# Kernel optimization log

Hardware: AMD Instinct MI355X
Metric: run time of the kernel (lower is better)

The kernel has to match this reference:

```python
import jax, jax.numpy as jnp
import numpy as np

B, NN, DEG = 64, 256, 8
N = B * NN
E = N * DEG
IN_N, IN_E = 128, 16
TOOL, PROC = 16, 12
TP = TOOL * PROC
H1 = 384

def _lin(key, i, o, s=0.05):
    k1, k2 = jax.random.split(key)
    return (jax.random.normal(k1, (i, o), jnp.float32) * s,
            jax.random.normal(k2, (o,), jnp.float32) * s)

def setup_inputs():
    ks = jax.random.split(jax.random.key(0), 40)
    inp = {}
    inp["ns"] = jax.random.normal(ks[0], (N, IN_N), jnp.float32)
    inp["es"] = jax.random.normal(ks[1], (E, IN_E), jnp.float32)
    inp["dm"] = jax.random.normal(ks[2], (N, NN), jnp.float32)
    inp["mask_fv"] = (jax.random.uniform(ks[3], (N, TP)) > 0.3).astype(jnp.float32)
    dst = jnp.repeat(jnp.arange(N, dtype=jnp.int32), DEG)  # fixed in-degree DEG
    src = (dst // NN) * NN + jax.random.randint(ks[4], (E,), 0, NN, dtype=jnp.int32)
    inp["src"], inp["dst"] = src, dst
    sizes = [(IN_N, H1), (H1 + 32, H1), (H1, TP)]
    for i, (cin, cout) in enumerate(sizes, 1):
        inp[f"Wm{i}"], inp[f"bm{i}"] = _lin(ks[5 + 3 * i], 2 * cin + IN_E, cin)
        inp[f"Wu{i}"], inp[f"bu{i}"] = _lin(ks[6 + 3 * i], 5 * cin, cout)
        inp[f"bng{i}"] = jnp.ones((cout,), jnp.float32)
        inp[f"bnb{i}"] = jnp.zeros((cout,), jnp.float32)
        inp[f"Wx{i}"], inp[f"bx{i}"] = _lin(ks[7 + 3 * i], cout, cout)
    inp["W1"], inp["b1"] = _lin(ks[20], NN, 64)
    inp["W2"], inp["b2"] = _lin(ks[21], 64, 32)
    inp["W3"], inp["b3"] = _lin(ks[22], NN, 64)
    inp["W4"], inp["b4"] = _lin(ks[23], 64, NN)
    return inp

def pna_conv(src, dst, h, e, Wm, bm, Wu, bu, bng, bnb, Wx, bx, relu_out):
    # DGL PNAConvTower: msg = M(cat(h_src, h_dst, e)); aggregate mean/max/sum/std per dst node;
    # U(cat(h, aggs)); BatchNorm (training stats); mixing Linear + LeakyReLU(0.01).
    cin = h.shape[1]
    msg = h[src] @ Wm[:cin] + h[dst] @ Wm[cin:2 * cin] + e @ Wm[2 * cin:] + bm  # [E, cin]
    cnt = jax.ops.segment_sum(jnp.ones((msg.shape[0],), msg.dtype), dst, N)[:, None]
    s = jax.ops.segment_sum(msg, dst, N)
    mean = s / cnt
    mx = jax.ops.segment_max(msg, dst, N)
    msq = jax.ops.segment_sum(msg * msg, dst, N) / cnt
    std = jnp.sqrt(jax.nn.relu(msq - mean * mean) + 1e-30)
    u = jnp.concatenate([h, mean, mx, s, std], axis=-1) @ Wu + bu  # [N, cout]
    u = (u - u.mean(0)) / jnp.sqrt(u.var(0) + 1e-5) * bng + bnb  # BatchNorm1d, training mode
    out = jax.nn.leaky_relu(u @ Wx + bx, 0.01)  # mixing layer
    return jax.nn.relu(out) if relu_out else out

def reference(ns, es, dm, mask_fv, Wm1, bm1, Wu1, bu1, bng1, bnb1, Wx1, bx1, Wm2, bm2, Wu2, bu2, bng2, bnb2, Wx2, bx2, Wm3, bm3, Wu3, bu3, bng3, bnb3, Wx3, bx3, W1, b1, W2, b2, W3, b3, W4, b4, src, dst):
    d2 = (dm @ W1 + b1) @ W2 + b2  # [N, 32]
    h1 = pna_conv(src, dst, ns, es, Wm1, bm1, Wu1, bu1, bng1, bnb1, Wx1, bx1, True)
    h2 = pna_conv(src, dst, jnp.concatenate([h1, d2], -1), es, Wm2, bm2, Wu2, bu2, bng2, bnb2, Wx2, bx2, True)
    h3 = pna_conv(src, dst, h2, es, Wm3, bm3, Wu3, bu3, bng3, bnb3, Wx3, bx3, False)  # [N, TP]
    nm = h3.max(-1).reshape(B, NN)
    g = jax.nn.sigmoid(jax.nn.relu(nm @ W3 + b3) @ W4 + b4)  # [B, NN]
    feat = (g.reshape(N, 1) * h3).reshape(B, -1)  # [B, NN*TP]
    feat = jnp.where(mask_fv.reshape(B, -1) == 0, -1e5, feat)
    return jax.nn.softmax(feat, -1)
```

## Files before the change

### kernel.cpp

```cpp
#include <hip/hip_runtime.h>
#include <hip/hip_bf16.h>

#define NNODE 16384

typedef short v8s __attribute__((ext_vector_type(8)));
typedef float v4f __attribute__((ext_vector_type(4)));
typedef unsigned short us16;

__device__ __forceinline__ us16 f2bf(float v) {
    unsigned u = __float_as_uint(v);
    unsigned r = (u + 0x7FFF + ((u >> 16) & 1)) >> 16;
    return (us16)r;
}
__device__ __forceinline__ float bf2f(us16 s) {
    return __uint_as_float(((unsigned)s) << 16);
}

template<int EPI, int OUT, int ACC, int BM>
__global__ __launch_bounds__(256, 4)
void mgemm5(const us16* __restrict__ Ah, const us16* __restrict__ Al,
            int ldA, int K,
            const us16* __restrict__ Bh, const us16* __restrict__ Bl, int KC,
            const float* __restrict__ CfIn, int ldCin,
            float* __restrict__ Cf, us16* __restrict__ Ch, us16* __restrict__ Cl,
            int ldC, int Ncol, const float* __restrict__ bias)
{
    constexpr int MF = BM / 32;
    __shared__ __align__(16) us16 AhS[BM * 64];
    __shared__ __align__(16) us16 AlS[BM * 64];
    const int bm = blockIdx.x * BM;
    const int bn = blockIdx.y * 64;
    const int tid = threadIdx.x;
    const int lane = tid & 63, wid = tid >> 6;
    const int wm = wid >> 1, wn = wid & 1;
    const int r16 = lane & 15, q = lane >> 4;
    v4f acc[MF][2];
#pragma unroll
    for (int i = 0; i < MF; i++)
#pragma unroll
        for (int j = 0; j < 2; j++) acc[i][j] = (v4f){0.f, 0.f, 0.f, 0.f};

    const int srow = tid >> 3;
    const int sc8  = tid & 7;
    const int cb0  = (bn >> 4) + wn * 2;
    const int nK = (K + 63) >> 6;
    for (int s = 0; s < nK; s++) {
        const int k0 = s << 6;
#pragma unroll
        for (int p = 0; p < BM / 32; p++) {
            int row = p * 32 + srow;
            size_t go = (size_t)(bm + row) * ldA + k0 + sc8 * 8;
            v8s hv = *(const v8s*)(const void*)(Ah + go);
            v8s lv = *(const v8s*)(const void*)(Al + go);
            int bo = row * 128 + ((sc8 * 16) ^ ((row & 7) << 4));
            *(v8s*)(void*)((char*)AhS + bo) = hv;
            *(v8s*)(void*)((char*)AlS + bo) = lv;
        }
        v8s Bfh[2][2], Bfl[2][2];
#pragma unroll
        for (int kc = 0; kc < 2; kc++) {
            int kchunk = (k0 >> 5) + kc;
#pragma unroll
            for (int nf = 0; nf < 2; nf++) {
                size_t fo = ((size_t)((cb0 + nf) * KC + kchunk) * 64 + lane) * 8;
                Bfh[kc][nf] = *(const v8s*)(const void*)(Bh + fo);
                Bfl[kc][nf] = *(const v8s*)(const void*)(Bl + fo);
            }
        }
        __syncthreads();
#pragma unroll
        for (int kc = 0; kc < 2; kc++) {
#pragma unroll
            for (int mf = 0; mf < MF; mf++) {
                int arow = wm * (BM / 2) + mf * 16 + r16;
                int ao = arow * 128 + (((kc * 64) + q * 16) ^ ((arow & 7) << 4));
                v8s ah = *(const v8s*)(const void*)((const char*)AhS + ao);
                v8s al = *(const v8s*)(const void*)((const char*)AlS + ao);
#pragma unroll
                for (int nf = 0; nf < 2; nf++) {
                    acc[mf][nf] = __builtin_amdgcn_mfma_f32_16x16x32_bf16(ah, Bfh[kc][nf], acc[mf][nf], 0, 0, 0);
                    acc[mf][nf] = __builtin_amdgcn_mfma_f32_16x16x32_bf16(al, Bfh[kc][nf], acc[mf][nf], 0, 0, 0);
                    acc[mf][nf] = __builtin_amdgcn_mfma_f32_16x16x32_bf16(ah, Bfl[kc][nf], acc[mf][nf], 0, 0, 0);
                }
            }
        }
        __syncthreads();
    }
#pragma unroll
    for (int mf = 0; mf < MF; mf++)
#pragma unroll
        for (int nf = 0; nf < 2; nf++) {
            int col = bn + wn * 32 + nf * 16 + r16;
            if (col < Ncol) {
                float bv = bias ? bias[col] : 0.f;
#pragma unroll
                for (int r = 0; r < 4; r++) {
                    int row = bm + wm * (BM / 2) + mf * 16 + q * 4 + r;
                    float v = acc[mf][nf][r] + bv;
                    if (ACC) v += CfIn[(size_t)row * ldCin + col];
                    if (EPI == 1) v = fmaxf(v, 0.f);
                    if (EPI == 2) v = (v > 0.f) ? v : 0.01f * v;
                    size_t o = (size_t)row * ldC + col;
                    if (OUT == 0) {
                        Cf[o] = v;
                    } else {
                        us16 h = f2bf(v);
                        Ch[o] = h;
                        Cl[o] = f2bf(v - bf2f(h));
                    }
                }
            }
        }
}

__global__ void prep_fr_bt(const float* __restrict__ W, int ldW,
                           us16* __restrict__ Bh, us16* __restrict__ Bl,
                           int K, int N, int KC)
{
    int idx = blockIdx.x * 256 + threadIdx.x;
    if (idx >= N * KC * 32) return;
    int e = idx & 7, lane = (idx >> 3) & 63, rem = idx >> 9;
    int kchunk = rem % KC, colblk = rem / KC;
    int n = colblk * 16 + (lane & 15);
    int k = kchunk * 32 + (lane >> 4) * 8 + e;
    float v = (k < K && n < N) ? W[(size_t)k * ldW + n] : 0.f;
    us16 h = f2bf(v);
    Bh[idx] = h;
    Bl[idx] = f2bf(v - bf2f(h));
}

__global__ void prep_fr_wu(const float* __restrict__ Wu,
                           us16* __restrict__ Bh, us16* __restrict__ Bl,
                           int cin, int cout, int KC)
{
    int idx = blockIdx.x * 256 + threadIdx.x;
    if (idx >= cout * KC * 32) return;
    int e = idx & 7, lane = (idx >> 3) & 63, rem = idx >> 9;
    int kchunk = rem % KC, colblk = rem / KC;
    int n = colblk * 16 + (lane & 15);
    int k = kchunk * 32 + (lane >> 4) * 8 + e;
    float v = 0.f;
    if (n < cout && k < 3 * cin) {
        if (k < cin)          v = Wu[(size_t)(cin + k) * cout + n] * 0.125f + Wu[(size_t)(3 * cin + k) * cout + n];
        else if (k < 2 * cin) v = Wu[(size_t)(2 * cin + (k - cin)) * cout + n];
        else                  v = Wu[(size_t)(4 * cin + (k - 2 * cin)) * cout + n];
    }
    us16 h = f2bf(v);
    Bh[idx] = h;
    Bl[idx] = f2bf(v - bf2f(h));
}

__global__ void prep_fr_wx(const float* __restrict__ Wx, const float* __restrict__ scale,
                           us16* __restrict__ Bh, us16* __restrict__ Bl,
                           int K, int N, int KC)
{
    int idx = blockIdx.x * 256 + threadIdx.x;
    if (idx >= N * KC * 32) return;
    int e = idx & 7, lane = (idx >> 3) & 63, rem = idx >> 9;
    int kchunk = rem % KC, colblk = rem / KC;
    int n = colblk * 16 + (lane & 15);
    int k = kchunk * 32 + (lane >> 4) * 8 + e;
    float v = (k < K && n < N) ? Wx[(size_t)k * N + n] * scale[k] : 0.f;
    us16 h = f2bf(v);
    Bh[idx] = h;
    Bl[idx] = f2bf(v - bf2f(h));
}

__global__ __launch_bounds__(256) void bias2p_k(const float* __restrict__ Wx,
    const float* __restrict__ bx, const float* __restrict__ shift,
    float* __restrict__ bias2, int K, int N)
{
    int n = blockIdx.x, tid = threadIdx.x;
    float s = 0.f;
    for (int k = tid; k < K; k += 256) s = fmaf(shift[k], Wx[(size_t)k * N + n], s);
    __shared__ float red[256];
    red[tid] = s; __syncthreads();
    for (int st = 128; st > 0; st >>= 1) { if (tid < st) red[tid] += red[tid + st]; __syncthreads(); }
    if (tid == 0) bias2[n] = red[0] + bx[n];
}

__global__ void prep_biasMU(const float* __restrict__ bm, const float* __restrict__ bu,
                            float* __restrict__ o, int cin, int cout)
{
    int i = blockIdx.x * 256 + threadIdx.x;
    if (i >= 2 * cin + cout) return;
    float v;
    if (i < cin)          v = 0.f;
    else if (i < 2 * cin) v = bm[i - cin];
    else                  v = bu[i - 2 * cin];
    o[i] = v;
}

__global__ void csplit_k(const float* __restrict__ src, int ldS, int w,
                         us16* __restrict__ Xh, us16* __restrict__ Xl,
                         int ldX, int offX)
{
    int idx = blockIdx.x * 256 + threadIdx.x;
    if (idx >= NNODE * w) return;
    int rrow = idx / w, c = idx - rrow * w;
    float v = src[(size_t)rrow * ldS + c];
    us16 h = f2bf(v);
    size_t o = (size_t)rrow * ldX + offX + c;
    Xh[o] = h;
    Xl[o] = f2bf(v - bf2f(h));
}

__global__ __launch_bounds__(256)
void gemm_k(const float* __restrict__ A, const float* __restrict__ Bw,
            float* __restrict__ C, int Ncol, int K, const float* __restrict__ bias)
{
    __shared__ float As[16][128];
    __shared__ float Bs[16][64];
    const int bm = blockIdx.y * 128;
    const int bn = blockIdx.x * 64;
    const int tid = threadIdx.x;
    const int tx = tid & 15, ty = tid >> 4;
    float acc[8][4];
#pragma unroll
    for (int i = 0; i < 8; i++)
#pragma unroll
        for (int j = 0; j < 4; j++) acc[i][j] = 0.f;

    for (int k0 = 0; k0 < K; k0 += 16) {
#pragma unroll
        for (int i = 0; i < 2; i++) {
            int idx = tid * 2 + i;
            int row = idx >> 2;
            int k4  = (idx & 3) << 2;
            const float* ap = A + (size_t)(bm + row) * K + k0 + k4;
            float4 v = *reinterpret_cast<const float4*>(ap);
            As[k4 + 0][row] = v.x;
            As[k4 + 1][row] = v.y;
            As[k4 + 2][row] = v.z;
            As[k4 + 3][row] = v.w;
        }
        {
            int row = tid >> 4;
            int c4  = (tid & 15) << 2;
            int gn  = bn + c4;
            float4 v;
            if (gn + 3 < Ncol) {
                v = *reinterpret_cast<const float4*>(Bw + (size_t)(k0 + row) * Ncol + gn);
            } else {
                float t0 = (gn + 0 < Ncol) ? Bw[(size_t)(k0 + row) * Ncol + gn + 0] : 0.f;
                float t1 = (gn + 1 < Ncol) ? Bw[(size_t)(k0 + row) * Ncol + gn + 1] : 0.f;
                float t2 = (gn + 2 < Ncol) ? Bw[(size_t)(k0 + row) * Ncol + gn + 2] : 0.f;
                float t3 = (gn + 3 < Ncol) ? Bw[(size_t)(k0 + row) * Ncol + gn + 3] : 0.f;
                v = make_float4(t0, t1, t2, t3);
            }
            *reinterpret_cast<float4*>(&Bs[row][c4]) = v;
        }
        __syncthreads();
#pragma unroll
        for (int kk = 0; kk < 16; kk++) {
            float a0[8], b0[4];
#pragma unroll
            for (int i = 0; i < 8; i++) a0[i] = As[kk][ty * 8 + i];
#pragma unroll
            for (int j = 0; j < 4; j++) b0[j] = Bs[kk][tx * 4 + j];
#pragma unroll
            for (int i = 0; i < 8; i++)
#pragma unroll
                for (int j = 0; j < 4; j++) acc[i][j] = fmaf(a0[i], b0[j], acc[i][j]);
        }
        __syncthreads();
    }
#pragma unroll
    for (int i = 0; i < 8; i++) {
        int r = bm + ty * 8 + i;
#pragma unroll
        for (int j = 0; j < 4; j++) {
            int c = bn + tx * 4 + j;
            if (c < Ncol) C[(size_t)r * Ncol + c] = acc[i][j] + (bias ? bias[c] : 0.f);
        }
    }
}

__global__ __launch_bounds__(256)
void agg2_k(const float* __restrict__ H2, const float* __restrict__ es,
            const int* __restrict__ src, const float* __restrict__ Wme,
            us16* __restrict__ Xh, us16* __restrict__ Xl,
            int cin, int ldH, int ldX, int offX)
{
    const int g = blockIdx.x;
    const int c0 = blockIdx.y * 64;
    const int qz = blockIdx.z;
    const int tid = threadIdx.x;
    const int nl = tid >> 6, c = tid & 63;
    const int cc = c0 + c;
    const bool act = cc < cin;
    __shared__ float esl[4][128];
    __shared__ int srcl[512];
    {
        int e0 = g * 2048 + qz * 512;
        for (int i = tid; i < 512; i += 256) srcl[i] = src[e0 + i] - g * 256;
    }
    float wreg[16];
#pragma unroll
    for (int j = 0; j < 16; j++) wreg[j] = act ? Wme[j * cin + cc] : 0.f;
    __syncthreads();
    const float* Hsrc = H2 + (size_t)(g * 256) * ldH + c0;
    const float* Hdst = H2 + (size_t)(g * 256) * ldH + cin + c0;
    for (int i = 0; i < 16; i++) {
        const int vl = qz * 64 + i * 4 + nl;
        {
            const float* ep = es + (size_t)(g * 256 + vl) * 128;
            esl[nl][c] = ep[c];
            esl[nl][64 + c] = ep[64 + c];
        }
        __syncthreads();
        if (act) {
            float hd = Hdst[(size_t)vl * ldH + c];
            float sum = 0.f, sq = 0.f, mx = -INFINITY;
#pragma unroll
            for (int e = 0; e < 8; e++) {
                int sl = srcl[(i * 4 + nl) * 8 + e];
                float m = hd + Hsrc[(size_t)sl * ldH + c];
                float4 e0 = *(const float4*)&esl[nl][e * 16 + 0];
                float4 e1 = *(const float4*)&esl[nl][e * 16 + 4];
                float4 e2 = *(const float4*)&esl[nl][e * 16 + 8];
                float4 e3 = *(const float4*)&esl[nl][e * 16 + 12];
                m = fmaf(e0.x, wreg[0], m);  m = fmaf(e0.y, wreg[1], m);
                m = fmaf(e0.z, wreg[2], m);  m = fmaf(e0.w, wreg[3], m);
                m = fmaf(e1.x, wreg[4], m);  m = fmaf(e1.y, wreg[5], m);
                m = fmaf(e1.z, wreg[6], m);  m = fmaf(e1.w, wreg[7], m);
                m = fmaf(e2.x, wreg[8], m);  m = fmaf(e2.y, wreg[9], m);
                m = fmaf(e2.z, wreg[10], m); m = fmaf(e2.w, wreg[11], m);
                m = fmaf(e3.x, wreg[12], m); m = fmaf(e3.y, wreg[13], m);
                m = fmaf(e3.z, wreg[14], m); m = fmaf(e3.w, wreg[15], m);
                sum += m;
                sq = fmaf(m, m, sq);
                mx = fmaxf(mx, m);
            }
            float mean = sum * 0.125f, msq = sq * 0.125f;
            float stdv = sqrtf(fmaxf(msq - mean * mean, 0.f) + 1e-30f);
            size_t o = (size_t)(g * 256 + vl) * ldX + offX + cc;
            us16 h;
            h = f2bf(sum);  Xh[o] = h;            Xl[o] = f2bf(sum - bf2f(h));
            h = f2bf(mx);   Xh[o + cin] = h;      Xl[o + cin] = f2bf(mx - bf2f(h));
            h = f2bf(stdv); Xh[o + 2 * cin] = h;  Xl[o + 2 * cin] = f2bf(stdv - bf2f(h));
        }
        __syncthreads();
    }
}

__global__ void bnstats1s_k(const us16* __restrict__ uh, const us16* __restrict__ ul,
                            float* __restrict__ part, int cout)
{
    int c = threadIdx.x;
    if (c >= cout) return;
    int r0 = blockIdx.x * 256;
    float s = 0.f, q = 0.f;
    for (int r = r0; r < r0 + 256; r++) {
        size_t o = (size_t)r * cout + c;
        float v = bf2f(uh[o]) + bf2f(ul[o]);
        s += v;
        q = fmaf(v, v, q);
    }
    part[(size_t)blockIdx.x * cout + c] = s;
    part[(size_t)(64 + blockIdx.x) * cout + c] = q;
}

__global__ void bnstats2_k(const float* __restrict__ part, const float* __restrict__ bng,
                           const float* __restrict__ bnb, float* __restrict__ scale,
                           float* __restrict__ shift, int cout)
{
    int c = threadIdx.x;
    if (c >= cout) return;
    float s = 0.f, q = 0.f;
    for (int b = 0; b < 64; b++) { s += part[(size_t)b * cout + c]; q += part[(size_t)(64 + b) * cout + c]; }
    float mean = s / 16384.f;
    float var  = q / 16384.f - mean * mean;
    float sc   = bng[c] / sqrtf(var + 1e-5f);
    scale[c] = sc;
    shift[c] = bnb[c] - mean * sc;
}

__global__ void rowmax_k(const float* __restrict__ h3, float* __restrict__ nm)
{
    int wave = threadIdx.x >> 6;
    int lane = threadIdx.x & 63;
    int node = blockIdx.x * 4 + wave;
    const float* row = h3 + (size_t)node * 192;
    float m = -INFINITY;
    for (int t = lane; t < 192; t += 64) m = fmaxf(m, row[t]);
#pragma unroll
    for (int off = 32; off > 0; off >>= 1) m = fmaxf(m, __shfl_down(m, off, 64));
    if (lane == 0) nm[node] = m;
}

__global__ __launch_bounds__(256) void g_k(const float* __restrict__ nm,
    const float* __restrict__ W3, const float* __restrict__ b3,
    const float* __restrict__ W4, const float* __restrict__ b4,
    float* __restrict__ g)
{
    __shared__ float row[256];
    __shared__ float t1[64];
    int b = blockIdx.x, tid = threadIdx.x;
    row[tid] = nm[b * 256 + tid];
    __syncthreads();
    if (tid < 64) {
        float a = b3[tid];
        for (int k = 0; k < 256; k++) a = fmaf(row[k], W3[k * 64 + tid], a);
        t1[tid] = fmaxf(a, 0.f);
    }
    __syncthreads();
    float a = b4[tid];
    for (int j = 0; j < 64; j++) a = fmaf(t1[j], W4[j * 256 + tid], a);
    g[b * 256 + tid] = 1.f / (1.f + expf(-a));
}

__global__ __launch_bounds__(256) void sm1_k(const float* __restrict__ mask,
    const float* __restrict__ g, const float* __restrict__ h3, float* __restrict__ part)
{
    int b = blockIdx.x, s = blockIdx.y, tid = threadIdx.x;
    float l[24];
#pragma unroll
    for (int t = 0; t < 24; t++) {
        int i = s * 6144 + t * 256 + tid;
        size_t idx = (size_t)b * 49152 + i;
        float mk = mask[idx];
        l[t] = (mk == 0.f) ? -1e5f : g[b * 256 + i / 192] * h3[idx];
    }
    float m = -INFINITY;
#pragma unroll
    for (int t = 0; t < 24; t++) m = fmaxf(m, l[t]);
    __shared__ float red[256];
    red[tid] = m; __syncthreads();
    for (int st = 128; st > 0; st >>= 1) { if (tid < st) red[tid] = fmaxf(red[tid], red[tid + st]); __syncthreads(); }
    m = red[0]; __syncthreads();
    float z = 0.f;
#pragma unroll
    for (int t = 0; t < 24; t++) z += expf(l[t] - m);
    red[tid] = z; __syncthreads();
    for (int st = 128; st > 0; st >>= 1) { if (tid < st) red[tid] += red[tid + st]; __syncthreads(); }
    if (tid == 0) { part[(b * 8 + s) * 2] = m; part[(b * 8 + s) * 2 + 1] = red[0]; }
}

__global__ void sm2_k(const float* __restrict__ part, float* __restrict__ mz)
{
    int b = threadIdx.x;
    if (b >= 64) return;
    float M = -INFINITY;
    for (int s = 0; s < 8; s++) M = fmaxf(M, part[(b * 8 + s) * 2]);
    float Z = 0.f;
    for (int s = 0; s < 8; s++) Z += part[(b * 8 + s) * 2 + 1] * expf(part[(b * 8 + s) * 2] - M);
    mz[b * 2] = M;
    mz[b * 2 + 1] = 1.f / Z;
}

__global__ __launch_bounds__(256) void sm3_k(const float* __restrict__ mask,
    const float* __restrict__ g, const float* __restrict__ h3,
    const float* __restrict__ mz, float* __restrict__ out)
{
    int b = blockIdx.x, s = blockIdx.y, tid = threadIdx.x;
    float M = mz[b * 2], invZ = mz[b * 2 + 1];
#pragma unroll
    for (int t = 0; t < 24; t++) {
        int i = s * 6144 + t * 256 + tid;
        size_t idx = (size_t)b * 49152 + i;
        float mk = mask[idx];
        float v = (mk == 0.f) ? -1e5f : g[b * 256 + i / 192] * h3[idx];
        out[idx] = expf(v - M) * invZ;
    }
}

extern "C" void kernel_launch(void* const* d_in, const int* in_sizes, int n_in,
                              void* d_out, int out_size, void* d_ws, size_t ws_size,
                              hipStream_t stream)
{
    const float* ns   = (const float*)d_in[0];
    const float* es   = (const float*)d_in[1];
    const float* dm   = (const float*)d_in[2];
    const float* mask = (const float*)d_in[3];
    const int*   src  = (const int*)d_in[4];
    const float* Wm1 = (const float*)d_in[6],  *bm1 = (const float*)d_in[7];
    const float* Wu1 = (const float*)d_in[8],  *bu1 = (const float*)d_in[9];
    const float* bng1= (const float*)d_in[10], *bnb1= (const float*)d_in[11];
    const float* Wx1 = (const float*)d_in[12], *bx1 = (const float*)d_in[13];
    const float* Wm2 = (const float*)d_in[14], *bm2 = (const float*)d_in[15];
    const float* Wu2 = (const float*)d_in[16], *bu2 = (const float*)d_in[17];
    const float* bng2= (const float*)d_in[18], *bnb2= (const float*)d_in[19];
    const float* Wx2 = (const float*)d_in[20], *bx2 = (const float*)d_in[21];
    const float* Wm3 = (const float*)d_in[22], *bm3 = (const float*)d_in[23];
    const float* Wu3 = (const float*)d_in[24], *bu3 = (const float*)d_in[25];
    const float* bng3= (const float*)d_in[26], *bnb3= (const float*)d_in[27];
    const float* Wx3 = (const float*)d_in[28], *bx3 = (const float*)d_in[29];
    const float* W1 = (const float*)d_in[30], *b1 = (const float*)d_in[31];
    const float* W2 = (const float*)d_in[32], *b2 = (const float*)d_in[33];
    const float* W3 = (const float*)d_in[34], *b3 = (const float*)d_in[35];
    const float* W4 = (const float*)d_in[36], *b4 = (const float*)d_in[37];
    float* out = (float*)d_out;

    const int N = NNODE;
    char* base = (char*)d_ws;
    size_t off = 0;
    auto alloc = [&](size_t bytes) -> void* {
        void* p = base + off;
        off = (off + bytes + 255) & ~(size_t)255;
        return p;
    };
    us16* Xh = (us16*)alloc((size_t)N * 1728 * 2);
    us16* Xl = (us16*)alloc((size_t)N * 1728 * 2);
    float* H2   = (float*)alloc((size_t)N * 1216 * 4);
    us16* uh = (us16*)alloc((size_t)N * 384 * 2);
    us16* ul = (us16*)alloc((size_t)N * 384 * 2);
    float* h3b  = (float*)alloc((size_t)N * 192 * 4);
    float* d2f  = (float*)alloc((size_t)N * 32 * 4);
    float* part = (float*)alloc((size_t)128 * 384 * 4);
    float* scale= (float*)alloc(384 * 4);
    float* shift= (float*)alloc(384 * 4);
    float* bias2= (float*)alloc(384 * 4);
    float* biasMU1 = (float*)alloc(640 * 4);
    float* biasMU2 = (float*)alloc(1216 * 4);
    float* biasMU3 = (float*)alloc(960 * 4);
    float* nm   = (float*)alloc((size_t)N * 4);
    float* gbuf = (float*)alloc((size_t)N * 4);
    float* smp  = (float*)alloc(64 * 8 * 2 * 4);
    float* smz  = (float*)alloc(64 * 2 * 4);
    auto aw = [&](size_t elems) -> us16* { return (us16*)alloc(elems * 2); };
    us16 *BM1h = aw((size_t)640 * 128),   *BM1l = aw((size_t)640 * 128);
    us16 *BA1h = aw((size_t)384 * 384),   *BA1l = aw((size_t)384 * 384);
    us16 *BX1h = aw((size_t)384 * 384),   *BX1l = aw((size_t)384 * 384);
    us16 *BM2h = aw((size_t)1216 * 448),  *BM2l = aw((size_t)1216 * 448);
    us16 *BA2h = aw((size_t)384 * 1280),  *BA2l = aw((size_t)384 * 1280);
    us16 *BX2h = aw((size_t)384 * 384),   *BX2l = aw((size_t)384 * 384);
    us16 *BM3h = aw((size_t)960 * 384),   *BM3l = aw((size_t)960 * 384);
    us16 *BA3h = aw((size_t)192 * 1152),  *BA3l = aw((size_t)192 * 1152);
    us16 *BX3h = aw((size_t)192 * 192),   *BX3l = aw((size_t)192 * 192);

    auto gp = [](size_t n) { return dim3((unsigned)((n + 255) / 256)); };
    auto fsec = [](us16* b, int c0, int KC) { return b + (size_t)(c0 / 16) * KC * 512; };

    prep_fr_bt<<<gp((size_t)128 * 128), 256, 0, stream>>>(Wm1,             128, fsec(BM1h, 0, 4),   fsec(BM1l, 0, 4),   128, 128, 4);
    prep_fr_bt<<<gp((size_t)128 * 128), 256, 0, stream>>>(Wm1 + 128 * 128, 128, fsec(BM1h, 128, 4), fsec(BM1l, 128, 4), 128, 128, 4);
    prep_fr_bt<<<gp((size_t)384 * 128), 256, 0, stream>>>(Wu1,             384, fsec(BM1h, 256, 4), fsec(BM1l, 256, 4), 128, 384, 4);
    prep_fr_wu<<<gp((size_t)384 * 384), 256, 0, stream>>>(Wu1, BA1h, BA1l, 128, 384, 12);
    prep_fr_bt<<<gp((size_t)416 * 448), 256, 0, stream>>>(Wm2,             416, fsec(BM2h, 0, 14),   fsec(BM2l, 0, 14),   416, 416, 14);
    prep_fr_bt<<<gp((size_t)416 * 448), 256, 0, stream>>>(Wm2 + 416 * 416, 416, fsec(BM2h, 416, 14), fsec(BM2l, 416, 14), 416, 416, 14);
    prep_fr_bt<<<gp((size_t)384 * 448), 256, 0, stream>>>(Wu2,             384, fsec(BM2h, 832, 14), fsec(BM2l, 832, 14), 416, 384, 14);
    prep_fr_wu<<<gp((size_t)384 * 1280), 256, 0, stream>>>(Wu2, BA2h, BA2l, 416, 384, 40);
    prep_fr_bt<<<gp((size_t)384 * 384), 256, 0, stream>>>(Wm3,             384, fsec(BM3h, 0, 12),   fsec(BM3l, 0, 12),   384, 384, 12);
    prep_fr_bt<<<gp((size_t)384 * 384), 256, 0, stream>>>(Wm3 + 384 * 384, 384, fsec(BM3h, 384, 12), fsec(BM3l, 384, 12), 384, 384, 12);
    prep_fr_bt<<<gp((size_t)192 * 384), 256, 0, stream>>>(Wu3,             192, fsec(BM3h, 768, 12), fsec(BM3l, 768, 12), 384, 192, 12);
    prep_fr_wu<<<gp((size_t)192 * 1152), 256, 0, stream>>>(Wu3, BA3h, BA3l, 384, 192, 36);
    prep_biasMU<<<gp(640), 256, 0, stream>>>(bm1, bu1, biasMU1, 128, 384);
    prep_biasMU<<<gp(1216), 256, 0, stream>>>(bm2, bu2, biasMU2, 416, 384);
    prep_biasMU<<<gp(960), 256, 0, stream>>>(bm3, bu3, biasMU3, 384, 192);

    csplit_k<<<gp((size_t)N * 128), 256, 0, stream>>>(ns, 128, 128, Xh, Xl, 512, 0);

    gemm_k<<<dim3(1, 128), 256, 0, stream>>>(dm, W1, H2, 64, 256, b1);
    gemm_k<<<dim3(1, 128), 256, 0, stream>>>(H2, W2, d2f, 32, 64, b2);

    mgemm5<0, 0, 0, 128><<<dim3(128, 10), 256, 0, stream>>>(Xh, Xl, 512, 128, BM1h, BM1l, 4,
        nullptr, 0, H2, nullptr, nullptr, 640, 640, biasMU1);
    agg2_k<<<dim3(64, 2, 4), 256, 0, stream>>>(H2, es, src, Wm1 + 2 * 128 * 128, Xh, Xl, 128, 640, 512, 128);
    mgemm5<0, 1, 1, 128><<<dim3(128, 6), 256, 0, stream>>>(Xh + 128, Xl + 128, 512, 384, BA1h, BA1l, 12,
        H2 + 256, 640, nullptr, uh, ul, 384, 384, nullptr);
    bnstats1s_k<<<64, 384, 0, stream>>>(uh, ul, part, 384);
    bnstats2_k<<<1, 384, 0, stream>>>(part, bng1, bnb1, scale, shift, 384);
    prep_fr_wx<<<gp((size_t)384 * 384), 256, 0, stream>>>(Wx1, scale, BX1h, BX1l, 384, 384, 12);
    bias2p_k<<<384, 256, 0, stream>>>(Wx1, bx1, shift, bias2, 384, 384);
    mgemm5<1, 1, 0, 128><<<dim3(128, 6), 256, 0, stream>>>(uh, ul, 384, 384, BX1h, BX1l, 12,
        nullptr, 0, nullptr, Xh, Xl, 1728, 384, bias2);
    csplit_k<<<gp((size_t)N * 32), 256, 0, stream>>>(d2f, 32, 32, Xh, Xl, 1728, 384);

    mgemm5<0, 0, 0, 128><<<dim3(128, 19), 256, 0, stream>>>(Xh, Xl, 1728, 416, BM2h, BM2l, 14,
        nullptr, 0, H2, nullptr, nullptr, 1216, 1216, biasMU2);
    agg2_k<<<dim3(64, 7, 4), 256, 0, stream>>>(H2, es, src, Wm2 + 2 * 416 * 416, Xh, Xl, 416, 1216, 1728, 416);
    mgemm5<0, 1, 1, 128><<<dim3(128, 6), 256, 0, stream>>>(Xh + 416, Xl + 416, 1728, 1248, BA2h, BA2l, 40,
        H2 + 832, 1216, nullptr, uh, ul, 384, 384, nullptr);
    bnstats1s_k<<<64, 384, 0, stream>>>(uh, ul, part, 384);
    bnstats2_k<<<1, 384, 0, stream>>>(part, bng2, bnb2, scale, shift, 384);
    prep_fr_wx<<<gp((size_t)384 * 384), 256, 0, stream>>>(Wx2, scale, BX2h, BX2l, 384, 384, 12);
    bias2p_k<<<384, 256, 0, stream>>>(Wx2, bx2, shift, bias2, 384, 384);
    mgemm5<1, 1, 0, 128><<<dim3(128, 6), 256, 0, stream>>>(uh, ul, 384, 384, BX2h, BX2l, 12,
        nullptr, 0, nullptr, Xh, Xl, 1536, 384, bias2);

    mgemm5<0, 0, 0, 128><<<dim3(128, 15), 256, 0, stream>>>(Xh, Xl, 1536, 384, BM3h, BM3l, 12,
        nullptr, 0, H2, nullptr, nullptr, 960, 960, biasMU3);
    agg2_k<<<dim3(64, 6, 4), 256, 0, stream>>>(H2, es, src, Wm3 + 2 * 384 * 384, Xh, Xl, 384, 960, 1536, 384);
    mgemm5<0, 1, 1, 64><<<dim3(256, 3), 256, 0, stream>>>(Xh + 384, Xl + 384, 1536, 1152, BA3h, BA3l, 36,
        H2 + 768, 960, nullptr, uh, ul, 192, 192, nullptr);
    bnstats1s_k<<<64, 384, 0, stream>>>(uh, ul, part, 192);
    bnstats2_k<<<1, 384, 0, stream>>>(part, bng3, bnb3, scale, shift, 192);
    prep_fr_wx<<<gp((size_t)192 * 192), 256, 0, stream>>>(Wx3, scale, BX3h, BX3l, 192, 192, 6);
    bias2p_k<<<192, 256, 0, stream>>>(Wx3, bx3, shift, bias2, 192, 192);
    mgemm5<2, 0, 0, 64><<<dim3(256, 3), 256, 0, stream>>>(uh, ul, 192, 192, BX3h, BX3l, 6,
        nullptr, 0, h3b, nullptr, nullptr, 192, 192, bias2);

    rowmax_k<<<N / 4, 256, 0, stream>>>(h3b, nm);
    g_k<<<64, 256, 0, stream>>>(nm, W3, b3, W4, b4, gbuf);
    sm1_k<<<dim3(64, 8), 256, 0, stream>>>(mask, gbuf, h3b, smp);
    sm2_k<<<1, 64, 0, stream>>>(smp, smz);
    sm3_k<<<dim3(64, 8), 256, 0, stream>>>(mask, gbuf, h3b, smz, out);
}
```

Before: 700.5 us.

## Widen GEMM column tiles, batch weight prep, fold dm MLP into MFMA GEMM

The MFMA GEMM gains an NB template parameter so one block covers 128 columns for the wide message GEMMs, reusing each staged A tile across more MFMAs and halving the grid's repeated A loads. Weight fragment preparation is merged into a single packed launch. W1·W2 is folded on device into one matrix so the dm projection runs as a single split-bf16 MFMA GEMM instead of two fp32 SIMT GEMMs. BN statistics use more blocks with shorter row ranges. Risks include higher register pressure from the doubled accumulators (launch bounds lowered to 3) and mode-2 descriptors that zero padding columns.

```diff
diff --git a/kernel.cpp b/kernel.cpp
--- a/kernel.cpp
+++ b/kernel.cpp
@@ -16,9 +16,9 @@
     return __uint_as_float(((unsigned)s) << 16);
 }
 
-template<int EPI, int OUT, int ACC, int BM>
-__global__ __launch_bounds__(256, 4)
-void mgemm5(const us16* __restrict__ Ah, const us16* __restrict__ Al,
+template<int EPI, int OUT, int ACC, int BM, int NB>
+__global__ __launch_bounds__(256, 3)
+void mgemm6(const us16* __restrict__ Ah, const us16* __restrict__ Al,
             int ldA, int K,
             const us16* __restrict__ Bh, const us16* __restrict__ Bl, int KC,
             const float* __restrict__ CfIn, int ldCin,
@@ -29,47 +29,54 @@
     __shared__ __align__(16) us16 AhS[BM * 64];
     __shared__ __align__(16) us16 AlS[BM * 64];
     const int bm = blockIdx.x * BM;
-    const int bn = blockIdx.y * 64;
+    const int bn0 = blockIdx.y * (64 * NB);
     const int tid = threadIdx.x;
     const int lane = tid & 63, wid = tid >> 6;
     const int wm = wid >> 1, wn = wid & 1;
     const int r16 = lane & 15, q = lane >> 4;
-    v4f acc[MF][2];
-#pragma unroll
-    for (int i = 0; i < MF; i++)
-#pragma unroll
-        for (int j = 0; j < 2; j++) acc[i][j] = (v4f){0.f, 0.f, 0.f, 0.f};
+    v4f acc[NB][MF][2];
+#pragma unroll
+    for (int b = 0; b < NB; b++)
+#pragma unroll
+        for (int i = 0; i < MF; i++)
+#pragma unroll
+            for (int j = 0; j < 2; j++) acc[b][i][j] = (v4f){0.f, 0.f, 0.f, 0.f};
 
     const int srow = tid >> 3;
     const int sc8  = tid & 7;
-    const int cb0  = (bn >> 4) + wn * 2;
+    const int cbw  = (bn0 >> 4) + wn * 2;
     const int nK = (K + 63) >> 6;
     for (int s = 0; s < nK; s++) {
         const int k0 = s << 6;
 #pragma unroll
         for (int p = 0; p < BM / 32; p++) {
             int row = p * 32 + srow;
-            size_t go = (size_t)(bm + row) * ldA + k0 + sc8 * 8;
-            v8s hv = *(const v8s*)(const void*)(Ah + go);
-            v8s lv = *(const v8s*)(const void*)(Al + go);
+            int gk = k0 + sc8 * 8;
+            v8s hv = (v8s){0,0,0,0,0,0,0,0};
+            v8s lv = (v8s){0,0,0,0,0,0,0,0};
+            if (gk < K) {
+                size_t go = (size_t)(bm + row) * ldA + gk;
+                hv = *(const v8s*)(const void*)(Ah + go);
+                lv = *(const v8s*)(const void*)(Al + go);
+            }
             int bo = row * 128 + ((sc8 * 16) ^ ((row & 7) << 4));
             *(v8s*)(void*)((char*)AhS + bo) = hv;
             *(v8s*)(void*)((char*)AlS + bo) = lv;
         }
-        v8s Bfh[2][2], Bfl[2][2];
+        __syncthreads();
 #pragma unroll
         for (int kc = 0; kc < 2; kc++) {
             int kchunk = (k0 >> 5) + kc;
-#pragma unroll
-            for (int nf = 0; nf < 2; nf++) {
-                size_t fo = ((size_t)((cb0 + nf) * KC + kchunk) * 64 + lane) * 8;
-                Bfh[kc][nf] = *(const v8s*)(const void*)(Bh + fo);
-                Bfl[kc][nf] = *(const v8s*)(const void*)(Bl + fo);
-            }
-        }
-        __syncthreads();
-#pragma unroll
-        for (int kc = 0; kc < 2; kc++) {
+            v8s bfh[NB][2], bfl[NB][2];
+#pragma unroll
+            for (int nb = 0; nb < NB; nb++)
+#pragma unroll
+                for (int nf = 0; nf < 2; nf++) {
+                    int colblk = cbw + nb * 4 + nf;
+                    size_t fo = ((size_t)(colblk * KC + kchunk) * 64 + lane) * 8;
+                    bfh[nb][nf] = *(const v8s*)(const void*)(Bh + fo);
+                    bfl[nb][nf] = *(const v8s*)(const void*)(Bl + fo);
+                }
 #pragma unroll
             for (int mf = 0; mf < MF; mf++) {
                 int arow = wm * (BM / 2) + mf * 16 + r16;
@@ -77,77 +84,80 @@
                 v8s ah = *(const v8s*)(const void*)((const char*)AhS + ao);
                 v8s al = *(const v8s*)(const void*)((const char*)AlS + ao);
 #pragma unroll
-                for (int nf = 0; nf < 2; nf++) {
-                    acc[mf][nf] = __builtin_amdgcn_mfma_f32_16x16x32_bf16(ah, Bfh[kc][nf], acc[mf][nf], 0, 0, 0);
-                    acc[mf][nf] = __builtin_amdgcn_mfma_f32_16x16x32_bf16(al, Bfh[kc][nf], acc[mf][nf], 0, 0, 0);
-                    acc[mf][nf] = __builtin_amdgcn_mfma_f32_16x16x32_bf16(ah, Bfl[kc][nf], acc[mf][nf], 0, 0, 0);
-                }
+                for (int nb = 0; nb < NB; nb++)
+#pragma unroll
+                    for (int nf = 0; nf < 2; nf++) {
+                        acc[nb][mf][nf] = __builtin_amdgcn_mfma_f32_16x16x32_bf16(ah, bfh[nb][nf], acc[nb][mf][nf], 0, 0, 0);
+                        acc[nb][mf][nf] = __builtin_amdgcn_mfma_f32_16x16x32_bf16(al, bfh[nb][nf], acc[nb][mf][nf], 0, 0, 0);
+                        acc[nb][mf][nf] = __builtin_amdgcn_mfma_f32_16x16x32_bf16(ah, bfl[nb][nf], acc[nb][mf][nf], 0, 0, 0);
+                    }
             }
         }
         __syncthreads();
     }
 #pragma unroll
-    for (int mf = 0; mf < MF; mf++)
-#pragma unroll
-        for (int nf = 0; nf < 2; nf++) {
-            int col = bn + wn * 32 + nf * 16 + r16;
-            if (col < Ncol) {
-                float bv = bias ? bias[col] : 0.f;
-#pragma unroll
-                for (int r = 0; r < 4; r++) {
-                    int row = bm + wm * (BM / 2) + mf * 16 + q * 4 + r;
-                    float v = acc[mf][nf][r] + bv;
-                    if (ACC) v += CfIn[(size_t)row * ldCin + col];
-                    if (EPI == 1) v = fmaxf(v, 0.f);
-                    if (EPI == 2) v = (v > 0.f) ? v : 0.01f * v;
-                    size_t o = (size_t)row * ldC + col;
-                    if (OUT == 0) {
-                        Cf[o] = v;
-                    } else {
-                        us16 h = f2bf(v);
-                        Ch[o] = h;
-                        Cl[o] = f2bf(v - bf2f(h));
+    for (int nb = 0; nb < NB; nb++)
+#pragma unroll
+        for (int mf = 0; mf < MF; mf++)
+#pragma unroll
+            for (int nf = 0; nf < 2; nf++) {
+                int col = bn0 + nb * 64 + wn * 32 + nf * 16 + r16;
+                if (col < Ncol) {
+                    float bv = bias ? bias[col] : 0.f;
+#pragma unroll
+                    for (int r = 0; r < 4; r++) {
+                        int row = bm + wm * (BM / 2) + mf * 16 + q * 4 + r;
+                        float v = acc[nb][mf][nf][r] + bv;
+                        if (ACC) v += CfIn[(size_t)row * ldCin + col];
+                        if (EPI == 1) v = fmaxf(v, 0.f);
+                        if (EPI == 2) v = (v > 0.f) ? v : 0.01f * v;
+                        size_t o = (size_t)row * ldC + col;
+                        if (OUT == 0) {
+                            Cf[o] = v;
+                        } else {
+                            us16 h = f2bf(v);
+                            Ch[o] = h;
+                            Cl[o] = f2bf(v - bf2f(h));
+                        }
                     }
                 }
             }
-        }
-}
-
-__global__ void prep_fr_bt(const float* __restrict__ W, int ldW,
-                           us16* __restrict__ Bh, us16* __restrict__ Bl,
-                           int K, int N, int KC)
-{
-    int idx = blockIdx.x * 256 + threadIdx.x;
-    if (idx >= N * KC * 32) return;
+}
+
+struct FrD {
+    const float* W;
+    us16* Bh;
+    us16* Bl;
+    int ldW, Kv, Nv, Na, KC, mode, cin, blk0;
+};
+struct FrPack { FrD d[16]; int nd; };
+
+__global__ __launch_bounds__(256) void prep_fr_all(FrPack p)
+{
+    int b = blockIdx.x;
+    int i = 0;
+    for (int j = 1; j < p.nd; j++) if (b >= p.d[j].blk0) i = j;
+    const FrD dd = p.d[i];
+    int idx = (b - dd.blk0) * 256 + threadIdx.x;
+    if (idx >= dd.Na * dd.KC * 32) return;
     int e = idx & 7, lane = (idx >> 3) & 63, rem = idx >> 9;
-    int kchunk = rem % KC, colblk = rem / KC;
-    int n = colblk * 16 + (lane & 15);
-    int k = kchunk * 32 + (lane >> 4) * 8 + e;
-    float v = (k < K && n < N) ? W[(size_t)k * ldW + n] : 0.f;
-    us16 h = f2bf(v);
-    Bh[idx] = h;
-    Bl[idx] = f2bf(v - bf2f(h));
-}
-
-__global__ void prep_fr_wu(const float* __restrict__ Wu,
-                           us16* __restrict__ Bh, us16* __restrict__ Bl,
-                           int cin, int cout, int KC)
-{
-    int idx = blockIdx.x * 256 + threadIdx.x;
-    if (idx >= cout * KC * 32) return;
-    int e = idx & 7, lane = (idx >> 3) & 63, rem = idx >> 9;
-    int kchunk = rem % KC, colblk = rem / KC;
+    int kchunk = rem % dd.KC, colblk = rem / dd.KC;
     int n = colblk * 16 + (lane & 15);
     int k = kchunk * 32 + (lane >> 4) * 8 + e;
     float v = 0.f;
-    if (n < cout && k < 3 * cin) {
-        if (k < cin)          v = Wu[(size_t)(cin + k) * cout + n] * 0.125f + Wu[(size_t)(3 * cin + k) * cout + n];
-        else if (k < 2 * cin) v = Wu[(size_t)(2 * cin + (k - cin)) * cout + n];
-        else                  v = Wu[(size_t)(4 * cin + (k - 2 * cin)) * cout + n];
+    if (dd.mode == 0) {
+        if (k < dd.Kv && n < dd.Nv) v = dd.W[(size_t)k * dd.ldW + n];
+    } else if (dd.mode == 1) {
+        int cin = dd.cin, cout = dd.Nv;
+        if (n < cout && k < 3 * cin) {
+            if (k < cin)          v = dd.W[(size_t)(cin + k) * cout + n] * 0.125f + dd.W[(size_t)(3 * cin + k) * cout + n];
+            else if (k < 2 * cin) v = dd.W[(size_t)(2 * cin + (k - cin)) * cout + n];
+            else                  v = dd.W[(size_t)(4 * cin + (k - 2 * cin)) * cout + n];
+        }
     }
     us16 h = f2bf(v);
-    Bh[idx] = h;
-    Bl[idx] = f2bf(v - bf2f(h));
+    dd.Bh[idx] = h;
+    dd.Bl[idx] = f2bf(v - bf2f(h));
 }
 
 __global__ void prep_fr_wx(const float* __restrict__ Wx, const float* __restrict__ scale,
@@ -166,6 +176,34 @@
     Bl[idx] = f2bf(v - bf2f(h));
 }
 
+__global__ void w12frag_k(const float* __restrict__ W1, const float* __restrict__ W2,
+                          us16* __restrict__ Bh, us16* __restrict__ Bl)
+{
+    int idx = blockIdx.x * 256 + threadIdx.x;
+    if (idx >= 64 * 8 * 32) return;
+    int e = idx & 7, lane = (idx >> 3) & 63, rem = idx >> 9;
+    int kchunk = rem % 8, colblk = rem / 8;
+    int n = colblk * 16 + (lane & 15);
+    int k = kchunk * 32 + (lane >> 4) * 8 + e;
+    float v = 0.f;
+    if (n < 32 && k < 256) {
+        for (int j = 0; j < 64; j++) v = fmaf(W1[(size_t)k * 64 + j], W2[(size_t)j * 32 + n], v);
+    }
+    us16 h = f2bf(v);
+    Bh[idx] = h;
+    Bl[idx] = f2bf(v - bf2f(h));
+}
+
+__global__ void bias12_k(const float* __restrict__ b1, const float* __restrict__ W2,
+                         const float* __restrict__ b2, float* __restrict__ b12)
+{
+    int n = threadIdx.x;
+    if (n >= 32) return;
+    float s = b2[n];
+    for (int j = 0; j < 64; j++) s = fmaf(b1[j], W2[(size_t)j * 32 + n], s);
+    b12[n] = s;
+}
+
 __global__ __launch_bounds__(256) void bias2p_k(const float* __restrict__ Wx,
     const float* __restrict__ bx, const float* __restrict__ shift,
     float* __restrict__ bias2, int K, int N)
@@ -189,6 +227,27 @@
     else if (i < 2 * cin) v = bm[i - cin];
     else                  v = bu[i - 2 * cin];
     o[i] = v;
+}
+
+__global__ void csplit2_k(const float* __restrict__ ns, us16* __restrict__ Xh, us16* __restrict__ Xl,
+                          const float* __restrict__ dm, us16* __restrict__ Dh, us16* __restrict__ Dl)
+{
+    int b = blockIdx.x;
+    if (b < 8192) {
+        int idx = b * 256 + threadIdx.x;
+        int rrow = idx >> 7, c = idx & 127;
+        float v = ns[idx];
+        us16 h = f2bf(v);
+        size_t o = (size_t)rrow * 512 + c;
+        Xh[o] = h;
+        Xl[o] = f2bf(v - bf2f(h));
+    } else {
+        int idx = (b - 8192) * 256 + threadIdx.x;
+        float v = dm[idx];
+        us16 h = f2bf(v);
+        Dh[idx] = h;
+        Dl[idx] = f2bf(v - bf2f(h));
+    }
 }
 
 __global__ void csplit_k(const float* __restrict__ src, int ldS, int w,
@@ -203,77 +262,6 @@
     size_t o = (size_t)rrow * ldX + offX + c;
     Xh[o] = h;
     Xl[o] = f2bf(v - bf2f(h));
-}
-
-__global__ __launch_bounds__(256)
-void gemm_k(const float* __restrict__ A, const float* __restrict__ Bw,
-            float* __restrict__ C, int Ncol, int K, const float* __restrict__ bias)
-{
-    __shared__ float As[16][128];
-    __shared__ float Bs[16][64];
-    const int bm = blockIdx.y * 128;
-    const int bn = blockIdx.x * 64;
-    const int tid = threadIdx.x;
-    const int tx = tid & 15, ty = tid >> 4;
-    float acc[8][4];
-#pragma unroll
-    for (int i = 0; i < 8; i++)
-#pragma unroll
-        for (int j = 0; j < 4; j++) acc[i][j] = 0.f;
-
-    for (int k0 = 0; k0 < K; k0 += 16) {
-#pragma unroll
-        for (int i = 0; i < 2; i++) {
-            int idx = tid * 2 + i;
-            int row = idx >> 2;
-            int k4  = (idx & 3) << 2;
-            const float* ap = A + (size_t)(bm + row) * K + k0 + k4;
-            float4 v = *reinterpret_cast<const float4*>(ap);
-            As[k4 + 0][row] = v.x;
-            As[k4 + 1][row] = v.y;
-            As[k4 + 2][row] = v.z;
-            As[k4 + 3][row] = v.w;
-        }
-        {
-            int row = tid >> 4;
-            int c4  = (tid & 15) << 2;
-            int gn  = bn + c4;
-            float4 v;
-            if (gn + 3 < Ncol) {
-                v = *reinterpret_cast<const float4*>(Bw + (size_t)(k0 + row) * Ncol + gn);
-            } else {
-                float t0 = (gn + 0 < Ncol) ? Bw[(size_t)(k0 + row) * Ncol + gn + 0] : 0.f;
-                float t1 = (gn + 1 < Ncol) ? Bw[(size_t)(k0 + row) * Ncol + gn + 1] : 0.f;
-                float t2 = (gn + 2 < Ncol) ? Bw[(size_t)(k0 + row) * Ncol + gn + 2] : 0.f;
-                float t3 = (gn + 3 < Ncol) ? Bw[(size_t)(k0 + row) * Ncol + gn + 3] : 0.f;
-                v = make_float4(t0, t1, t2, t3);
-            }
-            *reinterpret_cast<float4*>(&Bs[row][c4]) = v;
-        }
-        __syncthreads();
-#pragma unroll
-        for (int kk = 0; kk < 16; kk++) {
-            float a0[8], b0[4];
-#pragma unroll
-            for (int i = 0; i < 8; i++) a0[i] = As[kk][ty * 8 + i];
-#pragma unroll
-            for (int j = 0; j < 4; j++) b0[j] = Bs[kk][tx * 4 + j];
-#pragma unroll
-            for (int i = 0; i < 8; i++)
-#pragma unroll
-                for (int j = 0; j < 4; j++) acc[i][j] = fmaf(a0[i], b0[j], acc[i][j]);
-        }
-        __syncthreads();
-    }
-#pragma unroll
-    for (int i = 0; i < 8; i++) {
-        int r = bm + ty * 8 + i;
-#pragma unroll
-        for (int j = 0; j < 4; j++) {
-            int c = bn + tx * 4 + j;
-            if (c < Ncol) C[(size_t)r * Ncol + c] = acc[i][j] + (bias ? bias[c] : 0.f);
-        }
-    }
 }
 
 __global__ __launch_bounds__(256)
@@ -349,16 +337,16 @@
 {
     int c = threadIdx.x;
     if (c >= cout) return;
-    int r0 = blockIdx.x * 256;
+    int r0 = blockIdx.x * 64;
     float s = 0.f, q = 0.f;
-    for (int r = r0; r < r0 + 256; r++) {
+    for (int r = r0; r < r0 + 64; r++) {
         size_t o = (size_t)r * cout + c;
         float v = bf2f(uh[o]) + bf2f(ul[o]);
         s += v;
         q = fmaf(v, v, q);
     }
     part[(size_t)blockIdx.x * cout + c] = s;
-    part[(size_t)(64 + blockIdx.x) * cout + c] = q;
+    part[(size_t)(256 + blockIdx.x) * cout + c] = q;
 }
 
 __global__ void bnstats2_k(const float* __restrict__ part, const float* __restrict__ bng,
@@ -368,7 +356,7 @@
     int c = threadIdx.x;
     if (c >= cout) return;
     float s = 0.f, q = 0.f;
-    for (int b = 0; b < 64; b++) { s += part[(size_t)b * cout + c]; q += part[(size_t)(64 + b) * cout + c]; }
+    for (int b = 0; b < 256; b++) { s += part[(size_t)b * cout + c]; q += part[(size_t)(256 + b) * cout + c]; }
     float mean = s / 16384.f;
     float var  = q / 16384.f - mean * mean;
     float sc   = bng[c] / sqrtf(var + 1e-5f);
@@ -505,12 +493,15 @@
     float* H2   = (float*)alloc((size_t)N * 1216 * 4);
     us16* uh = (us16*)alloc((size_t)N * 384 * 2);
     us16* ul = (us16*)alloc((size_t)N * 384 * 2);
+    us16* dmh = (us16*)alloc((size_t)N * 256 * 2);
+    us16* dml = (us16*)alloc((size_t)N * 256 * 2);
     float* h3b  = (float*)alloc((size_t)N * 192 * 4);
     float* d2f  = (float*)alloc((size_t)N * 32 * 4);
-    float* part = (float*)alloc((size_t)128 * 384 * 4);
+    float* part = (float*)alloc((size_t)512 * 384 * 4);
     float* scale= (float*)alloc(384 * 4);
     float* shift= (float*)alloc(384 * 4);
     float* bias2= (float*)alloc(384 * 4);
+    float* b12  = (float*)alloc(32 * 4);
     float* biasMU1 = (float*)alloc(640 * 4);
     float* biasMU2 = (float*)alloc(1216 * 4);
     float* biasMU3 = (float*)alloc(960 * 4);
@@ -519,75 +510,89 @@
     float* smp  = (float*)alloc(64 * 8 * 2 * 4);
     float* smz  = (float*)alloc(64 * 2 * 4);
     auto aw = [&](size_t elems) -> us16* { return (us16*)alloc(elems * 2); };
-    us16 *BM1h = aw((size_t)640 * 128),   *BM1l = aw((size_t)640 * 128);
-    us16 *BA1h = aw((size_t)384 * 384),   *BA1l = aw((size_t)384 * 384);
-    us16 *BX1h = aw((size_t)384 * 384),   *BX1l = aw((size_t)384 * 384);
-    us16 *BM2h = aw((size_t)1216 * 448),  *BM2l = aw((size_t)1216 * 448);
-    us16 *BA2h = aw((size_t)384 * 1280),  *BA2l = aw((size_t)384 * 1280);
-    us16 *BX2h = aw((size_t)384 * 384),   *BX2l = aw((size_t)384 * 384);
-    us16 *BM3h = aw((size_t)960 * 384),   *BM3l = aw((size_t)960 * 384);
-    us16 *BA3h = aw((size_t)192 * 1152),  *BA3l = aw((size_t)192 * 1152);
-    us16 *BX3h = aw((size_t)192 * 192),   *BX3l = aw((size_t)192 * 192);
+    us16 *BM1h = aw((size_t)640 * 4 * 32),    *BM1l = aw((size_t)640 * 4 * 32);
+    us16 *BA1h = aw((size_t)384 * 12 * 32),   *BA1l = aw((size_t)384 * 12 * 32);
+    us16 *BX1h = aw((size_t)384 * 12 * 32),   *BX1l = aw((size_t)384 * 12 * 32);
+    us16 *BM2h = aw((size_t)1280 * 14 * 32),  *BM2l = aw((size_t)1280 * 14 * 32);
+    us16 *BA2h = aw((size_t)384 * 40 * 32),   *BA2l = aw((size_t)384 * 40 * 32);
+    us16 *BX2h = aw((size_t)384 * 12 * 32),   *BX2l = aw((size_t)384 * 12 * 32);
+    us16 *BM3h = aw((size_t)1024 * 12 * 32),  *BM3l = aw((size_t)1024 * 12 * 32);
+    us16 *BA3h = aw((size_t)192 * 36 * 32),   *BA3l = aw((size_t)192 * 36 * 32);
+    us16 *BX3h = aw((size_t)192 * 6 * 32),    *BX3l = aw((size_t)192 * 6 * 32);
+    us16 *B12h = aw((size_t)64 * 8 * 32),     *B12l = aw((size_t)64 * 8 * 32);
 
     auto gp = [](size_t n) { return dim3((unsigned)((n + 255) / 256)); };
     auto fsec = [](us16* b, int c0, int KC) { return b + (size_t)(c0 / 16) * KC * 512; };
 
-    prep_fr_bt<<<gp((size_t)128 * 128), 256, 0, stream>>>(Wm1,             128, fsec(BM1h, 0, 4),   fsec(BM1l, 0, 4),   128, 128, 4);
-    prep_fr_bt<<<gp((size_t)128 * 128), 256, 0, stream>>>(Wm1 + 128 * 128, 128, fsec(BM1h, 128, 4), fsec(BM1l, 128, 4), 128, 128, 4);
-    prep_fr_bt<<<gp((size_t)384 * 128), 256, 0, stream>>>(Wu1,             384, fsec(BM1h, 256, 4), fsec(BM1l, 256, 4), 128, 384, 4);
-    prep_fr_wu<<<gp((size_t)384 * 384), 256, 0, stream>>>(Wu1, BA1h, BA1l, 128, 384, 12);
-    prep_fr_bt<<<gp((size_t)416 * 448), 256, 0, stream>>>(Wm2,             416, fsec(BM2h, 0, 14),   fsec(BM2l, 0, 14),   416, 416, 14);
-    prep_fr_bt<<<gp((size_t)416 * 448), 256, 0, stream>>>(Wm2 + 416 * 416, 416, fsec(BM2h, 416, 14), fsec(BM2l, 416, 14), 416, 416, 14);
-    prep_fr_bt<<<gp((size_t)384 * 448), 256, 0, stream>>>(Wu2,             384, fsec(BM2h, 832, 14), fsec(BM2l, 832, 14), 416, 384, 14);
-    prep_fr_wu<<<gp((size_t)384 * 1280), 256, 0, stream>>>(Wu2, BA2h, BA2l, 416, 384, 40);
-    prep_fr_bt<<<gp((size_t)384 * 384), 256, 0, stream>>>(Wm3,             384, fsec(BM3h, 0, 12),   fsec(BM3l, 0, 12),   384, 384, 12);
-    prep_fr_bt<<<gp((size_t)384 * 384), 256, 0, stream>>>(Wm3 + 384 * 384, 384, fsec(BM3h, 384, 12), fsec(BM3l, 384, 12), 384, 384, 12);
-    prep_fr_bt<<<gp((size_t)192 * 384), 256, 0, stream>>>(Wu3,             192, fsec(BM3h, 768, 12), fsec(BM3l, 768, 12), 384, 192, 12);
-    prep_fr_wu<<<gp((size_t)192 * 1152), 256, 0, stream>>>(Wu3, BA3h, BA3l, 384, 192, 36);
+    FrPack pk;
+    int nd = 0, blk = 0;
+    auto addD = [&](const float* W, us16* Bh, us16* Bl, int ldW, int Kv, int Nv, int Na, int KC, int mode, int cin) {
+        pk.d[nd] = {W, Bh, Bl, ldW, Kv, Nv, Na, KC, mode, cin, blk};
+        blk += (Na * KC * 32 + 255) / 256;
+        nd++;
+    };
+    addD(Wm1,             fsec(BM1h,0,4),    fsec(BM1l,0,4),    128, 128, 128, 128, 4, 0, 0);
+    addD(Wm1 + 128*128,   fsec(BM1h,128,4),  fsec(BM1l,128,4),  128, 128, 128, 128, 4, 0, 0);
+    addD(Wu1,             fsec(BM1h,256,4),  fsec(BM1l,256,4),  384, 128, 384, 384, 4, 0, 0);
+    addD(Wu1,             BA1h, BA1l,        0,   0,   384, 384, 12, 1, 128);
+    addD(Wm2,             fsec(BM2h,0,14),   fsec(BM2l,0,14),   416, 416, 416, 416, 14, 0, 0);
+    addD(Wm2 + 416*416,   fsec(BM2h,416,14), fsec(BM2l,416,14), 416, 416, 416, 416, 14, 0, 0);
+    addD(Wu2,             fsec(BM2h,832,14), fsec(BM2l,832,14), 384, 416, 384, 384, 14, 0, 0);
+    addD(nullptr,         fsec(BM2h,1216,14),fsec(BM2l,1216,14),0,   0,   0,   64,  14, 2, 0);
+    addD(Wu2,             BA2h, BA2l,        0,   0,   384, 384, 40, 1, 416);
+    addD(Wm3,             fsec(BM3h,0,12),   fsec(BM3l,0,12),   384, 384, 384, 384, 12, 0, 0);
+    addD(Wm3 + 384*384,   fsec(BM3h,384,12), fsec(BM3l,384,12), 384, 384, 384, 384, 12, 0, 0);
+    addD(Wu3,             fsec(BM3h,768,12), fsec(BM3l,768,12), 192, 384, 192, 192, 12, 0, 0);
+    addD(nullptr,         fsec(BM3h,960,12), fsec(BM3l,960,12), 0,   0,   0,   64,  12, 2, 0);
+    addD(Wu3,             BA3h, BA3l,        0,   0,   192, 192, 36, 1, 384);
+    pk.nd = nd;
+
+    csplit2_k<<<8192 + 16384, 256, 0, stream>>>(ns, Xh, Xl, dm, dmh, dml);
+    prep_fr_all<<<blk, 256, 0, stream>>>(pk);
+    w12frag_k<<<gp(64 * 8 * 32), 256, 0, stream>>>(W1, W2, B12h, B12l);
+    bias12_k<<<1, 32, 0, stream>>>(b1, W2, b2, b12);
     prep_biasMU<<<gp(640), 256, 0, stream>>>(bm1, bu1, biasMU1, 128, 384);
     prep_biasMU<<<gp(1216), 256, 0, stream>>>(bm2, bu2, biasMU2, 416, 384);
     prep_biasMU<<<gp(960), 256, 0, stream>>>(bm3, bu3, biasMU3, 384, 192);
 
-    csplit_k<<<gp((size_t)N * 128), 256, 0, stream>>>(ns, 128, 128, Xh, Xl, 512, 0);
-
-    gemm_k<<<dim3(1, 128), 256, 0, stream>>>(dm, W1, H2, 64, 256, b1);
-    gemm_k<<<dim3(1, 128), 256, 0, stream>>>(H2, W2, d2f, 32, 64, b2);
-
-    mgemm5<0, 0, 0, 128><<<dim3(128, 10), 256, 0, stream>>>(Xh, Xl, 512, 128, BM1h, BM1l, 4,
+    mgemm6<0, 0, 0, 128, 1><<<dim3(128, 1), 256, 0, stream>>>(dmh, dml, 256, 256, B12h, B12l, 8,
+        nullptr, 0, d2f, nullptr, nullptr, 32, 32, b12);
+
+    mgemm6<0, 0, 0, 128, 2><<<dim3(128, 5), 256, 0, stream>>>(Xh, Xl, 512, 128, BM1h, BM1l, 4,
         nullptr, 0, H2, nullptr, nullptr, 640, 640, biasMU1);
     agg2_k<<<dim3(64, 2, 4), 256, 0, stream>>>(H2, es, src, Wm1 + 2 * 128 * 128, Xh, Xl, 128, 640, 512, 128);
-    mgemm5<0, 1, 1, 128><<<dim3(128, 6), 256, 0, stream>>>(Xh + 128, Xl + 128, 512, 384, BA1h, BA1l, 12,
+    mgemm6<0, 1, 1, 128, 1><<<dim3(128, 6), 256, 0, stream>>>(Xh + 128, Xl + 128, 512, 384, BA1h, BA1l, 12,
         H2 + 256, 640, nullptr, uh, ul, 384, 384, nullptr);
-    bnstats1s_k<<<64, 384, 0, stream>>>(uh, ul, part, 384);
+    bnstats1s_k<<<256, 384, 0, stream>>>(uh, ul, part, 384);
     bnstats2_k<<<1, 384, 0, stream>>>(part, bng1, bnb1, scale, shift, 384);
-    prep_fr_wx<<<gp((size_t)384 * 384), 256, 0, stream>>>(Wx1, scale, BX1h, BX1l, 384, 384, 12);
+    prep_fr_wx<<<gp((size_t)384 * 12 * 32), 256, 0, stream>>>(Wx1, scale, BX1h, BX1l, 384, 384, 12);
     bias2p_k<<<384, 256, 0, stream>>>(Wx1, bx1, shift, bias2, 384, 384);
-    mgemm5<1, 1, 0, 128><<<dim3(128, 6), 256, 0, stream>>>(uh, ul, 384, 384, BX1h, BX1l, 12,
+    mgemm6<1, 1, 0, 128, 1><<<dim3(128, 6), 256, 0, stream>>>(uh, ul, 384, 384, BX1h, BX1l, 12,
         nullptr, 0, nullptr, Xh, Xl, 1728, 384, bias2);
     csplit_k<<<gp((size_t)N * 32), 256, 0, stream>>>(d2f, 32, 32, Xh, Xl, 1728, 384);
 
-    mgemm5<0, 0, 0, 128><<<dim3(128, 19), 256, 0, stream>>>(Xh, Xl, 1728, 416, BM2h, BM2l, 14,
+    mgemm6<0, 0, 0, 128, 2><<<dim3(128, 10), 256, 0, stream>>>(Xh, Xl, 1728, 416, BM2h, BM2l, 14,
         nullptr, 0, H2, nullptr, nullptr, 1216, 1216, biasMU2);
     agg2_k<<<dim3(64, 7, 4), 256, 0, stream>>>(H2, es, src, Wm2 + 2 * 416 * 416, Xh, Xl, 416, 1216, 1728, 416);
-    mgemm5<0, 1, 1, 128><<<dim3(128, 6), 256, 0, stream>>>(Xh + 416, Xl + 416, 1728, 1248, BA2h, BA2l, 40,
+    mgemm6<0, 1, 1, 128, 1><<<dim3(128, 6), 256, 0, stream>>>(Xh + 416, Xl + 416, 1728, 1248, BA2h, BA2l, 40,
         H2 + 832, 1216, nullptr, uh, ul, 384, 384, nullptr);
-    bnstats1s_k<<<64, 384, 0, stream>>>(uh, ul, part, 384);
+    bnstats1s_k<<<256, 384, 0, stream>>>(uh, ul, part, 384);
     bnstats2_k<<<1, 384, 0, stream>>>(part, bng2, bnb2, scale, shift, 384);
-    prep_fr_wx<<<gp((size_t)384 * 384), 256, 0, stream>>>(Wx2, scale, BX2h, BX2l, 384, 384, 12);
+    prep_fr_wx<<<gp((size_t)384 * 12 * 32), 256, 0, stream>>>(Wx2, scale, BX2h, BX2l, 384, 384, 12);
     bias2p_k<<<384, 256, 0, stream>>>(Wx2, bx2, shift, bias2, 384, 384);
-    mgemm5<1, 1, 0, 128><<<dim3(128, 6), 256, 0, stream>>>(uh, ul, 384, 384, BX2h, BX2l, 12,
+    mgemm6<1, 1, 0, 128, 1><<<dim3(128, 6), 256, 0, stream>>>(uh, ul, 384, 384, BX2h, BX2l, 12,
         nullptr, 0, nullptr, Xh, Xl, 1536, 384, bias2);
 
-    mgemm5<0, 0, 0, 128><<<dim3(128, 15), 256, 0, stream>>>(Xh, Xl, 1536, 384, BM3h, BM3l, 12,
+    mgemm6<0, 0, 0, 128, 2><<<dim3(128, 8), 256, 0, stream>>>(Xh, Xl, 1536, 384, BM3h, BM3l, 12,
         nullptr, 0, H2, nullptr, nullptr, 960, 960, biasMU3);
     agg2_k<<<dim3(64, 6, 4), 256, 0, stream>>>(H2, es, src, Wm3 + 2 * 384 * 384, Xh, Xl, 384, 960, 1536, 384);
-    mgemm5<0, 1, 1, 64><<<dim3(256, 3), 256, 0, stream>>>(Xh + 384, Xl + 384, 1536, 1152, BA3h, BA3l, 36,
+    mgemm6<0, 1, 1, 64, 1><<<dim3(256, 3), 256, 0, stream>>>(Xh + 384, Xl + 384, 1536, 1152, BA3h, BA3l, 36,
         H2 + 768, 960, nullptr, uh, ul, 192, 192, nullptr);
-    bnstats1s_k<<<64, 384, 0, stream>>>(uh, ul, part, 192);
+    bnstats1s_k<<<256, 384, 0, stream>>>(uh, ul, part, 192);
     bnstats2_k<<<1, 384, 0, stream>>>(part, bng3, bnb3, scale, shift, 192);
-    prep_fr_wx<<<gp((size_t)192 * 192), 256, 0, stream>>>(Wx3, scale, BX3h, BX3l, 192, 192, 6);
+    prep_fr_wx<<<gp((size_t)192 * 6 * 32), 256, 0, stream>>>(Wx3, scale, BX3h, BX3l, 192, 192, 6);
     bias2p_k<<<192, 256, 0, stream>>>(Wx3, bx3, shift, bias2, 192, 192);
-    mgemm5<2, 0, 0, 64><<<dim3(256, 3), 256, 0, stream>>>(uh, ul, 192, 192, BX3h, BX3l, 6,
+    mgemm6<2, 0, 0, 64, 1><<<dim3(256, 3), 256, 0, stream>>>(uh, ul, 192, 192, BX3h, BX3l, 6,
         nullptr, 0, h3b, nullptr, nullptr, 192, 192, bias2);
 
     rowmax_k<<<N / 4, 256, 0, stream>>>(h3b, nm);
```

Measured after the change: 691.2 us. No clear change (-1.3%).
